# Kernel optimization log

Measured on AMD Instinct MI355X. Metric: run time of the kernel, lower is better.

Reference implementation:

```python
import jax, jax.numpy as jnp
import numpy as np

N, K, D = 16384, 32, 256
NEG_SLOPE = 0.01  # torch F.leaky_relu default


def setup_inputs() -> dict:
    key = jax.random.key(0)
    k1, k2, k3, k4 = jax.random.split(key, 4)
    scale = 1.0 / np.sqrt(D)
    return {
        "target": jax.random.normal(k1, (N, D), dtype=jnp.float32),
        "middle": jax.random.normal(k2, (N, K, D), dtype=jnp.float32),
        "W": jax.random.normal(k3, (D, D), dtype=jnp.float32) * scale,
        "b": jnp.zeros((D,), dtype=jnp.float32),
        "a_w": jax.random.normal(k4, (1, D), dtype=jnp.float32) * scale,
        "a_b": jnp.zeros((1,), dtype=jnp.float32),
    }


def reference(target, middle, W, b, a_w, a_b):
    # attention_weight applied to both target and middle (bias added to each,
    # matching the torch code which sums two Linear outputs)
    pt = target @ W.T + b              # [N, D]
    pm = middle @ W.T + b              # [N, K, D]
    h = pt[:, None, :] + pm            # [N, K, D]
    # a_weight: D -> 1
    score = h @ a_w.T + a_b            # [N, K, 1]
    score = jax.nn.leaky_relu(score, negative_slope=NEG_SLOPE)
    coef = jax.nn.softmax(score, axis=-2)   # softmax over neighbor dim K
    neighbor_feature = jnp.sum(coef * middle, axis=-2)  # [N, D]
    return neighbor_feature
```

## Files before the change

### kernel.cpp

```cpp
#include <hip/hip_runtime.h>

#define N_ 16384
#define K_ 32
#define D_ 256
#define NEG_SLOPE 0.01f

__global__ __launch_bounds__(1024) void prep_kernel(
    const float* __restrict__ W, const float* __restrict__ b,
    const float* __restrict__ a_w, const float* __restrict__ a_b,
    float* __restrict__ ws) {
  __shared__ float part[4][D_];
  __shared__ float sp[4];
  const int t = threadIdx.x;
  const int dd = t >> 8;
  const int e = t & 255;
  float acc = 0.f;
#pragma unroll 8
  for (int j = 0; j < 64; ++j) {
    const int d = dd * 64 + j;
    acc += a_w[d] * W[d * D_ + e];
  }
  part[dd][e] = acc;

  if (t < D_) {
    float s = b[t] * a_w[t];
#pragma unroll
    for (int off = 1; off < 64; off <<= 1) s += __shfl_xor(s, off);
    if ((t & 63) == 0) sp[t >> 6] = s;
  }
  __syncthreads();
  if (t < D_) ws[t] = part[0][t] + part[1][t] + part[2][t] + part[3][t];
  if (t == 0) ws[D_] = 2.f * (sp[0] + sp[1] + sp[2] + sp[3]) + a_b[0];
}

__global__ __launch_bounds__(512, 8) void attn_agg_kernel(
    const float* __restrict__ target, const float* __restrict__ middle,
    const float* __restrict__ ws, float* __restrict__ out) {
  __shared__ __align__(16) float part[8][D_];
  __shared__ float sdot[K_];
  __shared__ float stp[4];

  const int t = threadIdx.x;
  const int kg = t >> 6;
  const int l = t & 63;
  const int n = blockIdx.x;

  const float4* m4p = (const float4*)(middle + (size_t)n * K_ * D_);
  float4 m[4];
#pragma unroll
  for (int j = 0; j < 4; ++j) m[j] = m4p[(kg * 4 + j) * 64 + l];

  const float4 vv = ((const float4*)ws)[l];
  const float cadd = ws[D_];

  float pd[4];
#pragma unroll
  for (int j = 0; j < 4; ++j)
    pd[j] = m[j].x * vv.x + m[j].y * vv.y + m[j].z * vv.z + m[j].w * vv.w;
#pragma unroll
  for (int j = 0; j < 4; ++j) pd[j] += __shfl_xor(pd[j], 32);
  float q0 = (l & 32) ? pd[2] : pd[0];
  float q1 = (l & 32) ? pd[3] : pd[1];
  q0 += __shfl_xor(q0, 16);
  q1 += __shfl_xor(q1, 16);
  float r = (l & 16) ? q1 : q0;
  r += __shfl_xor(r, 8);
  r += __shfl_xor(r, 4);
  r += __shfl_xor(r, 2);
  r += __shfl_xor(r, 1);
  if ((l & 15) == 0)
    sdot[kg * 4 + ((l >> 5) * 2 + ((l >> 4) & 1))] = r;

  if (t < D_) {
    float tp = target[(size_t)n * D_ + t] * ws[t];
#pragma unroll
    for (int off = 1; off < 64; off <<= 1) tp += __shfl_xor(tp, off);
    if (l == 0) stp[kg] = tp;
  }
  __syncthreads();

  const float tdot = stp[0] + stp[1] + stp[2] + stp[3];
  float sc = sdot[l & 31] + tdot + cadd;
  sc = sc > 0.f ? sc : NEG_SLOPE * sc;
  float mx = sc;
  mx = fmaxf(mx, __shfl_xor(mx, 1));
  mx = fmaxf(mx, __shfl_xor(mx, 2));
  mx = fmaxf(mx, __shfl_xor(mx, 4));
  mx = fmaxf(mx, __shfl_xor(mx, 8));
  mx = fmaxf(mx, __shfl_xor(mx, 16));
  const float ex = __expf(sc - mx);
  float sm = ex;
  sm += __shfl_xor(sm, 1);
  sm += __shfl_xor(sm, 2);
  sm += __shfl_xor(sm, 4);
  sm += __shfl_xor(sm, 8);
  sm += __shfl_xor(sm, 16);
  const float coef = ex / sm;

  float4 acc = make_float4(0.f, 0.f, 0.f, 0.f);
#pragma unroll
  for (int j = 0; j < 4; ++j) {
    const float cf = __int_as_float(
        __builtin_amdgcn_readlane(__float_as_int(coef), kg * 4 + j));
    acc.x += cf * m[j].x;
    acc.y += cf * m[j].y;
    acc.z += cf * m[j].z;
    acc.w += cf * m[j].w;
  }
  *(float4*)(&part[kg][4 * l]) = acc;
  __syncthreads();

  if (t < 64) {
    float4 o = make_float4(0.f, 0.f, 0.f, 0.f);
#pragma unroll
    for (int w = 0; w < 8; ++w) {
      const float4 p = *(const float4*)(&part[w][4 * t]);
      o.x += p.x; o.y += p.y; o.z += p.z; o.w += p.w;
    }
    ((float4*)(out + (size_t)n * D_))[t] = o;
  }
}

extern "C" void kernel_launch(void* const* d_in, const int* in_sizes, int n_in,
                              void* d_out, int out_size, void* d_ws, size_t ws_size,
                              hipStream_t stream) {
  const float* target = (const float*)d_in[0];
  const float* middle = (const float*)d_in[1];
  const float* W      = (const float*)d_in[2];
  const float* b      = (const float*)d_in[3];
  const float* a_w    = (const float*)d_in[4];
  const float* a_b    = (const float*)d_in[5];
  float* out = (float*)d_out;
  float* ws  = (float*)d_ws;

  prep_kernel<<<1, 1024, 0, stream>>>(W, b, a_w, a_b, ws);
  attn_agg_kernel<<<N_, 512, 0, stream>>>(target, middle, ws, out);
}
```

Measured before the change: 108.4 us.

## Make attention kernel persistent with register double-buffered row prefetch

The grid shrinks from one block per row to a fixed 1024 blocks, each handling 16 consecutive rows. Each block keeps two register buffers so the global loads for the next row are in flight while the current row is reduced. The stock __syncthreads is replaced by a barrier that waits only on LDS counters, so outstanding global loads do not stall at each sync. The cost is higher register pressure and fewer resident rows per CU, which may reduce memory-level parallelism compared with the many small blocks used before.

Result: slower. 196.3 us (+81.1%).

```diff
diff --git a/kernel.cpp b/kernel.cpp
--- a/kernel.cpp
+++ b/kernel.cpp
@@ -4,6 +4,9 @@
 #define K_ 32
 #define D_ 256
 #define NEG_SLOPE 0.01f
+
+#define GRID_ 1024
+#define ITER_ 16
 
 __global__ __launch_bounds__(1024) void prep_kernel(
     const float* __restrict__ W, const float* __restrict__ b,
@@ -21,7 +24,6 @@
     acc += a_w[d] * W[d * D_ + e];
   }
   part[dd][e] = acc;
-
   if (t < D_) {
     float s = b[t] * a_w[t];
 #pragma unroll
@@ -33,30 +35,34 @@
   if (t == 0) ws[D_] = 2.f * (sp[0] + sp[1] + sp[2] + sp[3]) + a_b[0];
 }
 
-__global__ __launch_bounds__(512, 8) void attn_agg_kernel(
-    const float* __restrict__ target, const float* __restrict__ middle,
-    const float* __restrict__ ws, float* __restrict__ out) {
-  __shared__ __align__(16) float part[8][D_];
-  __shared__ float sdot[K_];
-  __shared__ float stp[4];
+struct MBuf {
+  float4 m[4];
+  float tg;
+};
 
-  const int t = threadIdx.x;
-  const int kg = t >> 6;
-  const int l = t & 63;
-  const int n = blockIdx.x;
+__device__ __forceinline__ void issue_loads(
+    MBuf& bf, const float* __restrict__ middle,
+    const float* __restrict__ target, int n, int kg, int l, int t) {
+  const float4* m4p = (const float4*)(middle + (size_t)n * K_ * D_);
+#pragma unroll
+  for (int j = 0; j < 4; ++j) bf.m[j] = m4p[(kg * 4 + j) * 64 + l];
+  bf.tg = target[(size_t)n * D_ + (t & 255)];
+}
 
-  const float4* m4p = (const float4*)(middle + (size_t)n * K_ * D_);
-  float4 m[4];
-#pragma unroll
-  for (int j = 0; j < 4; ++j) m[j] = m4p[(kg * 4 + j) * 64 + l];
+__device__ __forceinline__ void lgk_barrier() {
+  asm volatile("s_waitcnt lgkmcnt(0)" ::: "memory");
+  __builtin_amdgcn_s_barrier();
+}
 
-  const float4 vv = ((const float4*)ws)[l];
-  const float cadd = ws[D_];
-
+__device__ __forceinline__ void process(
+    const MBuf& bf, float (*part)[D_], float* sdot, float* stp,
+    const float4& vv, float vt, float cadd,
+    float* __restrict__ outrow, int t, int kg, int l) {
   float pd[4];
 #pragma unroll
   for (int j = 0; j < 4; ++j)
-    pd[j] = m[j].x * vv.x + m[j].y * vv.y + m[j].z * vv.z + m[j].w * vv.w;
+    pd[j] = bf.m[j].x * vv.x + bf.m[j].y * vv.y + bf.m[j].z * vv.z +
+            bf.m[j].w * vv.w;
 #pragma unroll
   for (int j = 0; j < 4; ++j) pd[j] += __shfl_xor(pd[j], 32);
   float q0 = (l & 32) ? pd[2] : pd[0];
@@ -72,12 +78,12 @@
     sdot[kg * 4 + ((l >> 5) * 2 + ((l >> 4) & 1))] = r;
 
   if (t < D_) {
-    float tp = target[(size_t)n * D_ + t] * ws[t];
+    float tp = bf.tg * vt;
 #pragma unroll
     for (int off = 1; off < 64; off <<= 1) tp += __shfl_xor(tp, off);
     if (l == 0) stp[kg] = tp;
   }
-  __syncthreads();
+  lgk_barrier();
 
   const float tdot = stp[0] + stp[1] + stp[2] + stp[3];
   float sc = sdot[l & 31] + tdot + cadd;
@@ -102,13 +108,13 @@
   for (int j = 0; j < 4; ++j) {
     const float cf = __int_as_float(
         __builtin_amdgcn_readlane(__float_as_int(coef), kg * 4 + j));
-    acc.x += cf * m[j].x;
-    acc.y += cf * m[j].y;
-    acc.z += cf * m[j].z;
-    acc.w += cf * m[j].w;
+    acc.x += cf * bf.m[j].x;
+    acc.y += cf * bf.m[j].y;
+    acc.z += cf * bf.m[j].z;
+    acc.w += cf * bf.m[j].w;
   }
   *(float4*)(&part[kg][4 * l]) = acc;
-  __syncthreads();
+  lgk_barrier();
 
   if (t < 64) {
     float4 o = make_float4(0.f, 0.f, 0.f, 0.f);
@@ -117,7 +123,38 @@
       const float4 p = *(const float4*)(&part[w][4 * t]);
       o.x += p.x; o.y += p.y; o.z += p.z; o.w += p.w;
     }
-    ((float4*)(out + (size_t)n * D_))[t] = o;
+    ((float4*)outrow)[t] = o;
+  }
+}
+
+__global__ __launch_bounds__(512, 8) void attn_agg_kernel(
+    const float* __restrict__ target, const float* __restrict__ middle,
+    const float* __restrict__ ws, float* __restrict__ out) {
+  __shared__ __align__(16) float part[8][D_];
+  __shared__ float sdot[K_];
+  __shared__ float stp[4];
+
+  const int t = threadIdx.x;
+  const int kg = t >> 6;
+  const int l = t & 63;
+  const int n0 = blockIdx.x * ITER_;
+
+  const float4 vv = ((const float4*)ws)[l];
+  const float vt = ws[t & 255];
+  const float cadd = ws[D_];
+
+  MBuf A, B;
+  issue_loads(A, middle, target, n0, kg, l, t);
+
+#pragma unroll 1
+  for (int it = 0; it < ITER_; it += 2) {
+    issue_loads(B, middle, target, n0 + it + 1, kg, l, t);
+    process(A, part, sdot, stp, vv, vt, cadd,
+            out + (size_t)(n0 + it) * D_, t, kg, l);
+    if (it + 2 < ITER_)
+      issue_loads(A, middle, target, n0 + it + 2, kg, l, t);
+    process(B, part, sdot, stp, vv, vt, cadd,
+            out + (size_t)(n0 + it + 1) * D_, t, kg, l);
   }
 }
 
@@ -134,5 +171,5 @@
   float* ws  = (float*)d_ws;
 
   prep_kernel<<<1, 1024, 0, stream>>>(W, b, a_w, a_b, ws);
-  attn_agg_kernel<<<N_, 512, 0, stream>>>(target, middle, ws, out);
+  attn_agg_kernel<<<GRID_, 512, 0, stream>>>(target, middle, ws, out);
 }
```
